# Performance work log

Measured on AMD Instinct MI355X. Metric: run time of the kernel, lower is better.

The kernel has to match this reference:

```python
import jax, jax.numpy as jnp
import numpy as np

T = 256          # trellis length (steps per sequence)
L = 16           # state bits
K = 2            # code bits per step
V = 2            # weights emitted per step
TLUT_BITS = 10   # LUT index bits
OUT, IN = 4096, 4096
NSEQ = (OUT * IN) // (T * V)      # 32768
CODES_PER_WORD = 32 // K          # 16


def fwht(x):
    """Normalized fast Walsh-Hadamard transform along the last axis (power-of-2)."""
    n = x.shape[-1]
    lead = x.shape[:-1]
    h = 1
    while h < n:
        x = x.reshape(lead + (n // (2 * h), 2, h))
        a, b = x[..., 0, :], x[..., 1, :]
        x = jnp.stack([a + b, a - b], axis=-2).reshape(lead + (n,))
        h *= 2
    return x / jnp.sqrt(jnp.asarray(n, x.dtype))


def decode_trellis(trellis, tlut):
    """Bit-unpack K-bit transition codes, run the L-bit shift-register trellis,
    and look up V weight values per state in the LUT."""
    t = jnp.arange(T)
    words = trellis[:, t // CODES_PER_WORD]            # [NSEQ, T] int32
    shifts = (32 - K) - K * (t % CODES_PER_WORD)       # MSB-first unpack
    codes = (words >> shifts) & (2 ** K - 1)           # [NSEQ, T]

    def step(state, code):
        state = ((state << K) | code) & (2 ** L - 1)
        return state, state

    _, states = jax.lax.scan(step, jnp.zeros(trellis.shape[0], jnp.int32),
                             codes.T.astype(jnp.int32))  # states: [T, NSEQ]
    states = states.T                                   # [NSEQ, T]
    vals = tlut[states & (2 ** TLUT_BITS - 1)]          # [NSEQ, T, V] LUT gather
    return vals.reshape(OUT, IN)


def incoherence_process(w_hat, SU, SV):
    """W = diag(SV) H_out  W_hat  H_in diag(SU)  (random-sign Hadamard)."""
    w = fwht(w_hat)        # Hadamard along in-dim
    w = fwht(w.T).T        # Hadamard along out-dim
    return w * SV[:, None] * SU[None, :]


def setup_inputs() -> dict:
    key = jax.random.key(0)
    ks = jax.random.split(key, 5)
    x = jax.random.normal(ks[0], (8192, IN), jnp.float32)
    trellis = jax.random.randint(ks[1], (NSEQ, 32 * T * K // (32 * 32)) if False else (NSEQ, (T * K) // 32), 0, 2147483647, dtype=jnp.int32)
    tlut = jax.random.normal(ks[2], (2 ** TLUT_BITS, V), jnp.float32)
    SU = jnp.sign(jax.random.normal(ks[3], (IN,), jnp.float32)) * 0.02
    SV = jnp.sign(jax.random.normal(ks[4], (OUT,), jnp.float32)) * 0.02
    return {"x": x, "trellis": trellis, "tlut": tlut, "SU": SU, "SV": SV}


def reference(x, trellis, tlut, SU, SV):
    w_hat = decode_trellis(trellis, tlut)       # [OUT, IN] dequantized weight
    w = incoherence_process(w_hat, SU, SV)      # Hadamard incoherence undo
    return x @ w.T                              # F.linear
```

## Files before the change

kernel.cpp:

```cpp
#include <hip/hip_runtime.h>
#include <hip/hip_bf16.h>
#include <stdint.h>

typedef __bf16 bf16x8 __attribute__((ext_vector_type(8)));
typedef float  f32x4  __attribute__((ext_vector_type(4)));

#define IN_DIM  4096
#define OUT_DIM 4096
#define M_DIM   8192

#define AS1 __attribute__((address_space(1)))
#define AS3 __attribute__((address_space(3)))

static __device__ __forceinline__ void gload_lds16(const void* g, void* l) {
  __builtin_amdgcn_global_load_lds((const AS1 void*)g, (AS3 void*)l, 16, 0, 0);
}
static __device__ __forceinline__ float bf2f(unsigned short u) {
  union { uint32_t i; float f; } c; c.i = (uint32_t)u << 16; return c.f;
}
static __device__ __forceinline__ unsigned short f2bf(float f) {
  __hip_bfloat16 h = __float2bfloat16(f); return *(const unsigned short*)&h;
}

__global__ __launch_bounds__(256) void k_decode_fwht_row(
    const int* __restrict__ trellis, const float2* __restrict__ tlut,
    const float* __restrict__ SU, __hip_bfloat16* __restrict__ w,
    const float* __restrict__ x, __hip_bfloat16* __restrict__ xb)
{
  __shared__ float buf[4096];
  __shared__ int words[128];
  __shared__ float2 lut[1024];
  const int tid = threadIdx.x;
  const int r = blockIdx.x;

  float4 xv[8];
  #pragma unroll
  for (int rep = 0; rep < 4; ++rep) {
    size_t i = (((size_t)r * 4 + rep) * 256 + tid) * 8;
    xv[rep * 2]     = *(const float4*)(x + i);
    xv[rep * 2 + 1] = *(const float4*)(x + i + 4);
  }

  if (tid < 128) words[tid] = trellis[r * 128 + tid];
  for (int i = tid; i < 1024; i += 256) lut[i] = tlut[i];
  __syncthreads();

  {
    const int t  = tid;
    const int wi = t >> 4;
    const int sh = 30 - 2 * (t & 15);
    const unsigned mask = (t < 4) ? ((1u << (2 * t + 2)) - 1u) : 1023u;
    #pragma unroll
    for (int s = 0; s < 8; ++s) {
      unsigned lo = (unsigned)words[s * 16 + wi];
      unsigned hi = wi ? (unsigned)words[s * 16 + wi - 1] : 0u;
      unsigned long long comb = ((unsigned long long)hi << 32) | (unsigned long long)lo;
      unsigned st = ((unsigned)(comb >> sh)) & mask;
      float2 v = lut[st];
      buf[s * 512 + 2 * t]     = v.x + v.y;
      buf[s * 512 + 2 * t + 1] = v.x - v.y;
    }
  }
  __syncthreads();

  for (int h = 2; h < 4096; h <<= 1) {
    #pragma unroll
    for (int q = 0; q < 8; ++q) {
      int b = q * 256 + tid;
      int i = ((b & ~(h - 1)) << 1) | (b & (h - 1));
      float a = buf[i], c = buf[i + h];
      buf[i]     = a + c;
      buf[i + h] = a - c;
    }
    __syncthreads();
  }

  for (int it2 = 0; it2 < 2; ++it2) {
    int c0 = (it2 * 256 + tid) * 8;
    union { unsigned short us[8]; uint4 v; } p;
    #pragma unroll
    for (int e = 0; e < 8; ++e)
      p.us[e] = f2bf(buf[c0 + e] * SU[c0 + e] * 0.015625f);
    *(uint4*)(w + (size_t)r * IN_DIM + c0) = p.v;
  }

  #pragma unroll
  for (int rep = 0; rep < 4; ++rep) {
    size_t i = (((size_t)r * 4 + rep) * 256 + tid) * 8;
    float4 v0 = xv[rep * 2], v1 = xv[rep * 2 + 1];
    union { __hip_bfloat16 h[8]; uint4 u; } p;
    p.h[0] = __float2bfloat16(v0.x); p.h[1] = __float2bfloat16(v0.y);
    p.h[2] = __float2bfloat16(v0.z); p.h[3] = __float2bfloat16(v0.w);
    p.h[4] = __float2bfloat16(v1.x); p.h[5] = __float2bfloat16(v1.y);
    p.h[6] = __float2bfloat16(v1.z); p.h[7] = __float2bfloat16(v1.w);
    *(uint4*)(xb + i) = p.u;
  }
}

__global__ __launch_bounds__(256) void k_fwht64_lo(__hip_bfloat16* __restrict__ w)
{
  __shared__ float tile[64][65];
  const int tid = threadIdx.x;
  const int rb = blockIdx.y, cb = blockIdx.x;

  for (int it = 0; it < 2; ++it) {
    int chunk = it * 256 + tid;
    int rr = chunk >> 3, jc = chunk & 7;
    uint4 v = *(const uint4*)(w + (size_t)(rb * 64 + rr) * IN_DIM + cb * 64 + jc * 8);
    const unsigned short* u = (const unsigned short*)&v;
    #pragma unroll
    for (int e = 0; e < 8; ++e) tile[rr][jc * 8 + e] = bf2f(u[e]);
  }
  __syncthreads();

  const int c = tid & 63, qf = tid >> 6;
  for (int h = 1; h < 64; h <<= 1) {
    #pragma unroll
    for (int u = 0; u < 8; ++u) {
      int b = qf * 8 + u;
      int i = ((b & ~(h - 1)) << 1) | (b & (h - 1));
      float a = tile[i][c], d = tile[i + h][c];
      tile[i][c]     = a + d;
      tile[i + h][c] = a - d;
    }
    __syncthreads();
  }

  for (int it = 0; it < 2; ++it) {
    int chunk = it * 256 + tid;
    int rr = chunk >> 3, jc = chunk & 7;
    union { unsigned short us[8]; uint4 v; } p;
    #pragma unroll
    for (int e = 0; e < 8; ++e) p.us[e] = f2bf(tile[rr][jc * 8 + e]);
    *(uint4*)(w + (size_t)(rb * 64 + rr) * IN_DIM + cb * 64 + jc * 8) = p.v;
  }
}

__global__ __launch_bounds__(256) void k_fwht64_hi(__hip_bfloat16* __restrict__ w,
                                                   const float* __restrict__ SV)
{
  __shared__ float tile[64][65];
  const int tid = threadIdx.x;
  const int r0 = blockIdx.y, cb = blockIdx.x;

  for (int it = 0; it < 2; ++it) {
    int chunk = it * 256 + tid;
    int r1 = chunk >> 3, jc = chunk & 7;
    uint4 v = *(const uint4*)(w + (size_t)(r0 + 64 * r1) * IN_DIM + cb * 64 + jc * 8);
    const unsigned short* u = (const unsigned short*)&v;
    #pragma unroll
    for (int e = 0; e < 8; ++e) tile[r1][jc * 8 + e] = bf2f(u[e]);
  }
  __syncthreads();

  const int c = tid & 63, qf = tid >> 6;
  for (int h = 1; h < 64; h <<= 1) {
    #pragma unroll
    for (int u = 0; u < 8; ++u) {
      int b = qf * 8 + u;
      int i = ((b & ~(h - 1)) << 1) | (b & (h - 1));
      float a = tile[i][c], d = tile[i + h][c];
      tile[i][c]     = a + d;
      tile[i + h][c] = a - d;
    }
    __syncthreads();
  }

  for (int it = 0; it < 2; ++it) {
    int chunk = it * 256 + tid;
    int r1 = chunk >> 3, jc = chunk & 7;
    int row = r0 + 64 * r1;
    float sv = SV[row] * 0.015625f;
    union { unsigned short us[8]; uint4 v; } p;
    #pragma unroll
    for (int e = 0; e < 8; ++e) p.us[e] = f2bf(tile[r1][jc * 8 + e] * sv);
    *(uint4*)(w + (size_t)row * IN_DIM + cb * 64 + jc * 8) = p.v;
  }
}

#define GBM 256
#define GBN 256
#define GBK 64
#define NT  (IN_DIM / GBK)

__global__ __launch_bounds__(512, 1) void k_gemm256(
    const __hip_bfloat16* __restrict__ X,
    const __hip_bfloat16* __restrict__ W,
    float* __restrict__ out)
{
  extern __shared__ __hip_bfloat16 smem[];
  __hip_bfloat16* As = smem;
  __hip_bfloat16* Bs = smem + 2 * 16384;

  const int tid  = threadIdx.x;
  const int lane = tid & 63;
  const int wave = tid >> 6;
  const int wm   = wave >> 2;
  const int wn   = wave & 3;
  const int lm   = lane & 15;
  const int lq   = lane >> 4;
  const int s_rw = tid >> 3;
  const int s_jj = tid & 7;

  const int nwg  = gridDim.x * gridDim.y;
  const int cpx  = nwg >> 3;
  const int orig = blockIdx.y * gridDim.x + blockIdx.x;
  const int swz  = (orig & 7) * cpx + (orig >> 3);
  const int bx   = swz % gridDim.x;
  const int by   = swz / gridDim.x;
  const int m0 = by * GBM, n0 = bx * GBN;

  f32x4 acc[8][4] = {};

#define STAGE_A(buf, u, kt) do {                                              \
    int row_ = (u) * 64 + s_rw;                                               \
    int js_  = s_jj ^ (row_ & 7);                                             \
    gload_lds16(X + (size_t)(m0 + row_) * IN_DIM + (kt) * GBK + js_ * 8,      \
                As + (buf) * 16384 + row_ * 64 + s_jj * 8);                   \
  } while (0)
#define STAGE_BE(buf, half, kt) do {                                          \
    int row_ = (half) * 128 + (s_rw & 31) + ((s_rw & 32) << 1);               \
    int js_  = s_jj ^ (row_ & 7);                                             \
    gload_lds16(W + (size_t)(n0 + row_) * IN_DIM + (kt) * GBK + js_ * 8,      \
                Bs + (buf) * 16384 + row_ * 64 + s_jj * 8);                   \
  } while (0)
#define STAGE_BL(buf, half, kt) do {                                          \
    int row_ = (half) * 128 + 32 + (s_rw & 31) + ((s_rw & 32) << 1);          \
    int js_  = s_jj ^ (row_ & 7);                                             \
    gload_lds16(W + (size_t)(n0 + row_) * IN_DIM + (kt) * GBK + js_ * 8,      \
                Bs + (buf) * 16384 + row_ * 64 + s_jj * 8);                   \
  } while (0)

#define RD_A_TO(DST, QM, BUF) do {                                            \
    const __hip_bfloat16* Ab_ = As + (BUF) * 16384;                           \
    _Pragma("unroll")                                                         \
    for (int mi2 = 0; mi2 < 4; ++mi2) {                                       \
      int r_ = wm * 128 + (QM) * 64 + mi2 * 16 + lm;                          \
      _Pragma("unroll")                                                       \
      for (int kk = 0; kk < 2; ++kk) {                                        \
        int q_ = kk * 4 + lq;                                                 \
        DST[mi2][kk] = *(const bf16x8*)(Ab_ + r_ * 64 + ((q_ ^ (r_ & 7)) << 3)); \
      }                                                                       \
    }                                                                         \
  } while (0)
#define RD_B_TO(DST, QN, BUF) do {                                            \
    const __hip_bfloat16* Bb_ = Bs + (BUF) * 16384;                           \
    _Pragma("unroll")                                                         \
    for (int ni2 = 0; ni2 < 2; ++ni2) {                                       \
      int r_ = wn * 64 + (QN) * 32 + ni2 * 16 + lm;                           \
      _Pragma("unroll")                                                       \
      for (int kk = 0; kk < 2; ++kk) {                                        \
        int q_ = kk * 4 + lq;                                                 \
        DST[ni2][kk] = *(const bf16x8*)(Bb_ + r_ * 64 + ((q_ ^ (r_ & 7)) << 3)); \
      }                                                                       \
    }                                                                         \
  } while (0)

#define FENCE asm volatile("" ::: "memory")
#define BAR do { FENCE; __builtin_amdgcn_s_barrier(); FENCE; } while (0)
#define VM4 do { asm volatile("s_waitcnt vmcnt(4)" ::: "memory"); } while (0)
#define MFMA_Q2(QM, QN, AF, BF) do {                                          \
    _Pragma("unroll")                                                         \
    for (int mi2 = 0; mi2 < 4; ++mi2)                                         \
      _Pragma("unroll")                                                       \
      for (int ni2 = 0; ni2 < 2; ++ni2)                                       \
        _Pragma("unroll")                                                     \
        for (int kk = 0; kk < 2; ++kk)                                        \
          acc[(QM) * 4 + mi2][(QN) * 2 + ni2] =                               \
              __builtin_amdgcn_mfma_f32_16x16x32_bf16(                        \
                  AF[mi2][kk], BF[ni2][kk],                                   \
                  acc[(QM) * 4 + mi2][(QN) * 2 + ni2], 0, 0, 0);              \
  } while (0)

  bf16x8 aE0[4][2], b00a[2][2];

  STAGE_BE(0, 0, 0); STAGE_BE(0, 1, 0);
  STAGE_A (0, 0, 0); STAGE_A (0, 2, 0);
  STAGE_BL(0, 0, 0); STAGE_BL(0, 1, 0);
  STAGE_A (0, 1, 0); STAGE_A (0, 3, 0);
  STAGE_A (1, 0, 1); STAGE_A (1, 2, 1);
  STAGE_BL(1, 0, 1); STAGE_BL(1, 1, 1);
  STAGE_A (1, 1, 1); STAGE_A (1, 3, 1);
  asm volatile("s_waitcnt vmcnt(6)" ::: "memory");
  BAR;
  RD_A_TO(aE0, 0, 0); RD_B_TO(b00a, 0, 0);

  for (int it = 0; it < NT / 2; ++it) {
    const int t1 = 2 * it + 1;
    const int t2 = (2 * it + 2 < NT) ? 2 * it + 2 : NT - 1;
    const int t3 = (2 * it + 3 < NT) ? 2 * it + 3 : NT - 1;

    bf16x8 aO0[4][2], aE1[4][2], aO1[4][2];
    bf16x8 b10[2][2], b00b[2][2], b01a[2][2], b11[2][2], b01b[2][2];

    BAR;
    STAGE_BE(1, 0, t1); STAGE_BE(1, 1, t1);
    __builtin_amdgcn_s_setprio(1);
    RD_B_TO(b10, 1, 0);
    MFMA_Q2(0, 0, aE0, b00a);
    __builtin_amdgcn_s_setprio(0);

    BAR;
    STAGE_A(0, 0, t2); STAGE_A(0, 2, t2);
    __builtin_amdgcn_s_setprio(1);
    RD_A_TO(aO0, 1, 0);
    MFMA_Q2(0, 1, aE0, b10);
    __builtin_amdgcn_s_setprio(0);

    BAR;
    STAGE_BL(0, 0, t2); STAGE_BL(0, 1, t2);
    __builtin_amdgcn_s_setprio(1);
    RD_B_TO(b00b, 0, 0);
    MFMA_Q2(1, 1, aO0, b10);
    __builtin_amdgcn_s_setprio(0);
    VM4;

    BAR;
    STAGE_A(0, 1, t2); STAGE_A(0, 3, t2);
    __builtin_amdgcn_s_setprio(1);
    RD_A_TO(aE1, 0, 1); RD_B_TO(b01a, 0, 1);
    MFMA_Q2(1, 0, aO0, b00b);
    __builtin_amdgcn_s_setprio(0);

    BAR;
    STAGE_BE(0, 0, t2); STAGE_BE(0, 1, t2);
    __builtin_amdgcn_s_setprio(1);
    RD_B_TO(b11, 1, 1);
    MFMA_Q2(0, 0, aE1, b01a);
    __builtin_amdgcn_s_setprio(0);

    BAR;
    STAGE_A(1, 0, t3); STAGE_A(1, 2, t3);
    __builtin_amdgcn_s_setprio(1);
    RD_A_TO(aO1, 1, 1);
    MFMA_Q2(0, 1, aE1, b11);
    __builtin_amdgcn_s_setprio(0);

    BAR;
    STAGE_BL(1, 0, t3); STAGE_BL(1, 1, t3);
    __builtin_amdgcn_s_setprio(1);
    RD_B_TO(b01b, 0, 1);
    MFMA_Q2(1, 1, aO1, b11);
    __builtin_amdgcn_s_setprio(0);
    VM4;

    BAR;
    STAGE_A(1, 1, t3); STAGE_A(1, 3, t3);
    __builtin_amdgcn_s_setprio(1);
    RD_A_TO(aE0, 0, 0); RD_B_TO(b00a, 0, 0);
    MFMA_Q2(1, 0, aO1, b01b);
    __builtin_amdgcn_s_setprio(0);
  }

  asm volatile("s_waitcnt vmcnt(0)" ::: "memory");

  #pragma unroll
  for (int mi = 0; mi < 8; ++mi) {
    #pragma unroll
    for (int ni = 0; ni < 4; ++ni) {
      int col   = n0 + wn * 64 + ni * 16 + lm;
      int rbase = m0 + wm * 128 + mi * 16 + lq * 4;
      #pragma unroll
      for (int rg = 0; rg < 4; ++rg) {
        out[(size_t)(rbase + rg) * OUT_DIM + col] = acc[mi][ni][rg];
      }
    }
  }
#undef MFMA_Q2
#undef VM4
#undef BAR
#undef FENCE
#undef RD_B_TO
#undef RD_A_TO
#undef STAGE_BL
#undef STAGE_BE
#undef STAGE_A
}

extern "C" void kernel_launch(void* const* d_in, const int* in_sizes, int n_in,
                              void* d_out, int out_size, void* d_ws, size_t ws_size,
                              hipStream_t stream) {
  (void)in_sizes; (void)n_in; (void)out_size; (void)ws_size;
  const float* x       = (const float*)d_in[0];
  const int*   trellis = (const int*)d_in[1];
  const float* tlut    = (const float*)d_in[2];
  const float* SU      = (const float*)d_in[3];
  const float* SV      = (const float*)d_in[4];
  float* out = (float*)d_out;

  __hip_bfloat16* Wd = (__hip_bfloat16*)d_ws;
  __hip_bfloat16* Xb = (__hip_bfloat16*)((char*)d_ws + (size_t)32 * 1024 * 1024);

  k_decode_fwht_row<<<4096, 256, 0, stream>>>(trellis, (const float2*)tlut, SU, Wd, x, Xb);
  k_fwht64_lo<<<dim3(64, 64), 256, 0, stream>>>(Wd);
  k_fwht64_hi<<<dim3(64, 64), 256, 0, stream>>>(Wd, SV);

  hipFuncSetAttribute((const void*)k_gemm256,
                      hipFuncAttributeMaxDynamicSharedMemorySize, 131072);
  k_gemm256<<<dim3(IN_DIM / GBN, M_DIM / GBM), 512, 131072, stream>>>(Xb, Wd, out);
}
```

Measured before the change: 324.1 us.

## Use radix-4 FWHT butterflies, register-level early stages, and XCD-tiled GEMM block mapping

The row FWHT now runs its first butterfly stages (the pair and the stride-512 slices) in registers before writing to LDS, then does the remaining stages as radix-4 passes. This halves the number of LDS round trips and __syncthreads barriers. The 64-point column FWHT kernels also switch to radix-4 passes. Separately, the GEMM block swizzle now maps each XCD's blocks to an 8x8 sub-tile of the output grid to improve L2 reuse, but this hardcodes a 16x32 grid shape. The register-level stages add register pressure in the decode kernel.

```diff
diff --git a/kernel.cpp b/kernel.cpp
--- a/kernel.cpp
+++ b/kernel.cpp
@@ -45,6 +45,7 @@
   for (int i = tid; i < 1024; i += 256) lut[i] = tlut[i];
   __syncthreads();
 
+  float y[8][2];
   {
     const int t  = tid;
     const int wi = t >> 4;
@@ -57,20 +58,43 @@
       unsigned long long comb = ((unsigned long long)hi << 32) | (unsigned long long)lo;
       unsigned st = ((unsigned)(comb >> sh)) & mask;
       float2 v = lut[st];
-      buf[s * 512 + 2 * t]     = v.x + v.y;
-      buf[s * 512 + 2 * t + 1] = v.x - v.y;
-    }
+      y[s][0] = v.x + v.y;
+      y[s][1] = v.x - v.y;
+    }
+  }
+  #pragma unroll
+  for (int st = 1; st < 8; st <<= 1) {
+    #pragma unroll
+    for (int s = 0; s < 8; ++s) {
+      if (!(s & st)) {
+        #pragma unroll
+        for (int j = 0; j < 2; ++j) {
+          float a = y[s][j], b = y[s | st][j];
+          y[s][j]      = a + b;
+          y[s | st][j] = a - b;
+        }
+      }
+    }
+  }
+  #pragma unroll
+  for (int s = 0; s < 8; ++s) {
+    buf[s * 512 + 2 * tid]     = y[s][0];
+    buf[s * 512 + 2 * tid + 1] = y[s][1];
   }
   __syncthreads();
 
-  for (int h = 2; h < 4096; h <<= 1) {
-    #pragma unroll
-    for (int q = 0; q < 8; ++q) {
-      int b = q * 256 + tid;
-      int i = ((b & ~(h - 1)) << 1) | (b & (h - 1));
-      float a = buf[i], c = buf[i + h];
-      buf[i]     = a + c;
-      buf[i + h] = a - c;
+  #pragma unroll
+  for (int h = 2; h <= 128; h <<= 2) {
+    #pragma unroll
+    for (int p = 0; p < 4; ++p) {
+      int q = p * 256 + tid;
+      int i = ((q & ~(h - 1)) << 2) | (q & (h - 1));
+      float p0 = buf[i], p1 = buf[i + h], p2 = buf[i + 2 * h], p3 = buf[i + 3 * h];
+      float a = p0 + p1, b = p0 - p1, c2 = p2 + p3, d = p2 - p3;
+      buf[i]         = a + c2;
+      buf[i + h]     = b + d;
+      buf[i + 2 * h] = a - c2;
+      buf[i + 3 * h] = b - d;
     }
     __syncthreads();
   }
@@ -114,14 +138,19 @@
   __syncthreads();
 
   const int c = tid & 63, qf = tid >> 6;
-  for (int h = 1; h < 64; h <<= 1) {
-    #pragma unroll
-    for (int u = 0; u < 8; ++u) {
-      int b = qf * 8 + u;
-      int i = ((b & ~(h - 1)) << 1) | (b & (h - 1));
-      float a = tile[i][c], d = tile[i + h][c];
-      tile[i][c]     = a + d;
-      tile[i + h][c] = a - d;
+  #pragma unroll
+  for (int h = 1; h <= 16; h <<= 2) {
+    #pragma unroll
+    for (int u = 0; u < 4; ++u) {
+      int q = qf * 4 + u;
+      int i = ((q & ~(h - 1)) << 2) | (q & (h - 1));
+      float p0 = tile[i][c], p1 = tile[i + h][c];
+      float p2 = tile[i + 2 * h][c], p3 = tile[i + 3 * h][c];
+      float a = p0 + p1, b = p0 - p1, cc = p2 + p3, d = p2 - p3;
+      tile[i][c]         = a + cc;
+      tile[i + h][c]     = b + d;
+      tile[i + 2 * h][c] = a - cc;
+      tile[i + 3 * h][c] = b - d;
     }
     __syncthreads();
   }
@@ -154,14 +183,19 @@
   __syncthreads();
 
   const int c = tid & 63, qf = tid >> 6;
-  for (int h = 1; h < 64; h <<= 1) {
-    #pragma unroll
-    for (int u = 0; u < 8; ++u) {
-      int b = qf * 8 + u;
-      int i = ((b & ~(h - 1)) << 1) | (b & (h - 1));
-      float a = tile[i][c], d = tile[i + h][c];
-      tile[i][c]     = a + d;
-      tile[i + h][c] = a - d;
+  #pragma unroll
+  for (int h = 1; h <= 16; h <<= 2) {
+    #pragma unroll
+    for (int u = 0; u < 4; ++u) {
+      int q = qf * 4 + u;
+      int i = ((q & ~(h - 1)) << 2) | (q & (h - 1));
+      float p0 = tile[i][c], p1 = tile[i + h][c];
+      float p2 = tile[i + 2 * h][c], p3 = tile[i + 3 * h][c];
+      float a = p0 + p1, b = p0 - p1, cc = p2 + p3, d = p2 - p3;
+      tile[i][c]         = a + cc;
+      tile[i + h][c]     = b + d;
+      tile[i + 2 * h][c] = a - cc;
+      tile[i + 3 * h][c] = b - d;
     }
     __syncthreads();
   }
@@ -202,12 +236,11 @@
   const int s_rw = tid >> 3;
   const int s_jj = tid & 7;
 
-  const int nwg  = gridDim.x * gridDim.y;
-  const int cpx  = nwg >> 3;
   const int orig = blockIdx.y * gridDim.x + blockIdx.x;
-  const int swz  = (orig & 7) * cpx + (orig >> 3);
-  const int bx   = swz % gridDim.x;
-  const int by   = swz / gridDim.x;
+  const int c8   = orig & 7;
+  const int idx  = orig >> 3;
+  const int bx   = (c8 & 1) * 8 + (idx & 7);
+  const int by   = (c8 >> 1) * 8 + (idx >> 3);
   const int m0 = by * GBM, n0 = bx * GBN;
 
   f32x4 acc[8][4] = {};
```

After: 304.5 us. 6.0% less time.
